# Optimization experiments

Measured on AMD Instinct MI355X. Metric: run time of the kernel, lower is better.

Reference implementation:

```python
import jax, jax.numpy as jnp
from jax import lax
import numpy as np

B, T, N, F_IN, H, E, K = 8, 32, 500, 64, 128, 8000, 3
LN_EPS = 1e-5


def setup_inputs() -> dict:
    key = jax.random.key(0)
    ks = jax.random.split(key, 10)
    x = jax.random.normal(ks[0], (B, T, N, F_IN), dtype=jnp.float32)
    edge_index = jax.random.randint(ks[1], (2, E), 0, N, dtype=jnp.int64)
    edge_weight = jax.random.uniform(ks[2], (E,), dtype=jnp.float32)
    # GCNConv: linear (in->out) + bias
    W_gcn = jax.random.normal(ks[3], (F_IN, H), dtype=jnp.float32) / np.sqrt(F_IN)
    b_gcn = jnp.zeros((H,), dtype=jnp.float32)
    # Conv1d(H, H, K): weight (O, I, K)
    W_temp = jax.random.normal(ks[4], (H, H, K), dtype=jnp.float32) / np.sqrt(H * K)
    b_temp = jnp.zeros((H,), dtype=jnp.float32)
    # LayerNorm(H)
    ln_w = jnp.ones((H,), dtype=jnp.float32)
    ln_b = jnp.zeros((H,), dtype=jnp.float32)
    # residual Linear (in->out)
    W_res = jax.random.normal(ks[5], (F_IN, H), dtype=jnp.float32) / np.sqrt(F_IN)
    b_res = jnp.zeros((H,), dtype=jnp.float32)
    return {"x": x, "edge_index": edge_index, "edge_weight": edge_weight,
            "W_gcn": W_gcn, "b_gcn": b_gcn, "W_temp": W_temp, "b_temp": b_temp,
            "ln_w": ln_w, "ln_b": ln_b, "W_res": W_res, "b_res": b_res}


def reference(x, edge_index, edge_weight, W_gcn, b_gcn, W_temp, b_temp, ln_w, ln_b, W_res, b_res):
    Bv, Tv, Nv, Fv = x.shape
    Hv = W_gcn.shape[1]
    res = x @ W_res + b_res  # (B,T,N,H)

    # ---- spatial GCNConv on B*T replicated graphs (vectorized, no index offsetting) ----
    xf = x.reshape(Bv * Tv, Nv, Fv) @ W_gcn  # (BT,N,H)
    src, dst = edge_index[0], edge_index[1]
    loops = jnp.arange(Nv, dtype=edge_index.dtype)
    src2 = jnp.concatenate([src, loops])
    dst2 = jnp.concatenate([dst, loops])
    ew2 = jnp.concatenate([edge_weight, jnp.ones((Nv,), dtype=edge_weight.dtype)])
    deg = jax.ops.segment_sum(ew2, dst2, num_segments=Nv)
    dinv = jnp.where(deg > 0, deg ** -0.5, 0.0)
    norm = dinv[src2] * ew2 * dinv[dst2]  # (E+N,)
    msgs = xf[:, src2, :] * norm[None, :, None]  # (BT, E+N, H)
    agg = jax.vmap(lambda m: jax.ops.segment_sum(m, dst2, num_segments=Nv))(msgs)
    h = jax.nn.gelu(agg + b_gcn, approximate=False)  # (BT,N,H)

    # ---- temporal Conv1d over T ----
    h = h.reshape(Bv, Tv, Nv, Hv).transpose(0, 2, 3, 1).reshape(Bv * Nv, Hv, Tv)
    pad = K // 2
    h = lax.conv_general_dilated(h, W_temp, window_strides=(1,), padding=[(pad, pad)],
                                 dimension_numbers=("NCH", "OIH", "NCH"))
    h = jax.nn.gelu(h + b_temp[None, :, None], approximate=False)
    h = h.reshape(Bv, Nv, Hv, Tv).transpose(0, 3, 1, 2)  # (B,T,N,H)

    # ---- fused residual + LayerNorm over last dim ----
    y = h + res
    mu = jnp.mean(y, axis=-1, keepdims=True)
    var = jnp.mean((y - mu) ** 2, axis=-1, keepdims=True)
    return (y - mu) * lax.rsqrt(var + LN_EPS) * ln_w + ln_b
```

## Files before the change

kernel.cpp:

```cpp
#include <hip/hip_runtime.h>
#include <hip/hip_bf16.h>
#include <math.h>

#define Bv 8
#define Tv 32
#define Nv 500
#define Fin 64
#define Hv 128
#define Ev 8000
#define Kv 3
#define BT (Bv*Tv)
#define ROWS (BT*Nv)
#define TP (Tv+2)
#define KK (Kv*Hv)
#define LDSROW 144

typedef __attribute__((ext_vector_type(8))) short s8v;
typedef __attribute__((ext_vector_type(4))) float f4v;

__device__ __forceinline__ float gelu_exact(float v){
    return 0.5f*v*(1.0f + erff(v*0.70710678118654752440f));
}
__device__ __forceinline__ short f2bs(float f){
    union { __hip_bfloat16 h; short s; } u;
    u.h = __float2bfloat16(f);
    return u.s;
}
__device__ __forceinline__ float b2f(short s){
    union { unsigned int i; float f; } u;
    u.i = ((unsigned int)(unsigned short)s) << 16;
    return u.f;
}

__global__ __launch_bounds__(1024) void k_prep(const int* __restrict__ ei,
        const float* __restrict__ ew, float* __restrict__ dinv,
        int* __restrict__ offs, int* __restrict__ csrc, float* __restrict__ cw){
    __shared__ float sdeg[Nv];
    __shared__ int   scnt[Nv];
    __shared__ float sdv[Nv];
    __shared__ int   scur[Nv];
    __shared__ int   sa[512], sb[512];
    int tid = threadIdx.x;
    if (tid < Nv){ sdeg[tid] = 1.0f; scnt[tid] = 0; }
    __syncthreads();
    for (int e = tid; e < Ev; e += 1024){
        int d = ei[Ev + e];
        atomicAdd(&sdeg[d], ew[e]);
        atomicAdd(&scnt[d], 1);
    }
    __syncthreads();
    int c = 0;
    if (tid < Nv){
        float d = sdeg[tid];
        float v = (d > 0.f) ? rsqrtf(d) : 0.f;
        sdv[tid] = v; dinv[tid] = v;
    }
    if (tid < 512){ c = (tid < Nv) ? scnt[tid] : 0; sa[tid] = c; }
    __syncthreads();
    int* s = sa; int* t = sb;
    for (int off = 1; off < 512; off <<= 1){
        int v = 0;
        if (tid < 512){ v = s[tid]; if (tid >= off) v += s[tid - off]; }
        if (tid < 512) t[tid] = v;
        __syncthreads();
        int* tmp = s; s = t; t = tmp;
    }
    if (tid < Nv){ int excl = s[tid] - c; offs[tid] = excl; scur[tid] = excl; }
    if (tid == 0) offs[Nv] = Ev;
    __syncthreads();
    for (int e = tid; e < Ev; e += 1024){
        int sn = ei[e], d = ei[Ev + e];
        int pos = atomicAdd(&scur[d], 1);
        csrc[pos] = sn;
        cw[pos] = sdv[sn]*ew[e]*sdv[d];
    }
}

__global__ __launch_bounds__(256) void k_xpose(const float* __restrict__ x,
        short* __restrict__ X2b, const float* __restrict__ W,
        const float* __restrict__ Wg, const float* __restrict__ Wr,
        short* __restrict__ W2, short* __restrict__ Wgt, short* __restrict__ Wrt){
    int bid = blockIdx.x;
    if (bid < ROWS/16){
        int gid = bid*256 + threadIdx.x;
        int row = gid >> 4, c4 = gid & 15;
        int bt = row / Nv;
        int n  = row - bt*Nv;
        float4 v = ((const float4*)x)[gid];
        short4 sv;
        sv.x = f2bs(v.x); sv.y = f2bs(v.y); sv.z = f2bs(v.z); sv.w = f2bs(v.w);
        *(short4*)(X2b + (size_t)n*(BT*64) + bt*64 + c4*4) = sv;
    } else {
        int idx = (bid - ROWS/16)*256 + threadIdx.x;
        if (idx < Hv*Hv*Kv){
            int o = idx/(Hv*Kv);
            int rem = idx - o*(Hv*Kv);
            int i = rem/Kv, k = rem - i*Kv;
            W2[o*KK + k*Hv + i] = f2bs(W[idx]);
        } else if (idx < Hv*Hv*Kv + Hv*64){
            int j = idx - Hv*Hv*Kv;
            int o = j >> 6, k = j & 63;
            Wgt[j] = f2bs(Wg[k*Hv + o]);
        } else if (idx < Hv*Hv*Kv + 2*Hv*64){
            int j = idx - Hv*Hv*Kv - Hv*64;
            int o = j >> 6, k = j & 63;
            Wrt[j] = f2bs(Wr[k*Hv + o]);
        }
    }
}

__global__ __launch_bounds__(256) void k_spmm(const short* __restrict__ X2b,
        const float* __restrict__ dinv, const int* __restrict__ offs,
        const int* __restrict__ csrc, const float* __restrict__ cw,
        short* __restrict__ AGG2){
    int bid = blockIdx.x;
    int ct = bid / Nv;
    int n  = bid - ct*Nv;
    int col = ct*2048 + threadIdx.x*8;
    float dv = dinv[n];
    float sw = dv*dv;
    float acc[8];
    s8v v = *(const s8v*)(X2b + (size_t)n*(BT*64) + col);
    #pragma unroll
    for (int q = 0; q < 8; ++q) acc[q] = sw * b2f(v[q]);
    int e0 = offs[n], e1 = offs[n+1];
    for (int e = e0; e < e1; ++e){
        int s = csrc[e]; float w = cw[e];
        s8v u = *(const s8v*)(X2b + (size_t)s*(BT*64) + col);
        #pragma unroll
        for (int q = 0; q < 8; ++q) acc[q] = fmaf(w, b2f(u[q]), acc[q]);
    }
    s8v r;
    #pragma unroll
    for (int q = 0; q < 8; ++q) r[q] = f2bs(acc[q]);
    *(s8v*)(AGG2 + (size_t)n*(BT*64) + col) = r;
}

__global__ __launch_bounds__(256, 2) void k_mega(
        const short* __restrict__ AGG2, const short* __restrict__ X2b,
        const short* __restrict__ W2, const short* __restrict__ Wgt,
        const short* __restrict__ Wrt,
        const float* __restrict__ bg, const float* __restrict__ btm,
        const float* __restrict__ br, const float* __restrict__ lw,
        const float* __restrict__ lb, float* __restrict__ out){
    __shared__ short hs[4*TP*LDSROW];
    __shared__ float red[Tv][4][2];
    int tid  = threadIdx.x;
    int w    = tid >> 6;
    int lane = tid & 63;
    int quad = lane >> 4;
    int laneo = lane & 15;
    int bid = blockIdx.x;
    int b  = bid / 125;
    int n0 = (bid - b*125) * 4;
    int o_base = w*32;

    float bgv[2], bbv[2], brv[2], lwv[2], lbv[2];
    #pragma unroll
    for (int nt = 0; nt < 2; ++nt){
        int o = o_base + nt*16 + laneo;
        bgv[nt] = bg[o]; bbv[nt] = btm[o]; brv[nt] = br[o];
        lwv[nt] = lw[o]; lbv[nt] = lb[o];
    }

    s8v bwg[2][2];
    #pragma unroll
    for (int nt = 0; nt < 2; ++nt){
        const short* wp = Wgt + (o_base + nt*16 + laneo)*64 + quad*8;
        bwg[nt][0] = *(const s8v*)wp;
        bwg[nt][1] = *(const s8v*)(wp + 32);
    }

    if (tid < 128){
        int node = tid >> 5, rem = tid & 31;
        int tp = (rem >> 4)*(TP-1), c8 = rem & 15;
        s8v z = {0,0,0,0,0,0,0,0};
        *(s8v*)&hs[node*(TP*LDSROW) + tp*LDSROW + c8*8] = z;
    }

    for (int g = 0; g < 4; ++g){
        int n = n0 + g;
        const short* ap = AGG2 + ((size_t)n*BT + b*Tv)*64;
        #pragma unroll
        for (int m = 0; m < 2; ++m){
            const short* arp = ap + (m*16 + laneo)*64 + quad*8;
            s8v a0 = *(const s8v*)arp;
            s8v a1 = *(const s8v*)(arp + 32);
            f4v h0 = {0.f,0.f,0.f,0.f}, h1 = {0.f,0.f,0.f,0.f};
            h0 = __builtin_amdgcn_mfma_f32_16x16x32_bf16(a0, bwg[0][0], h0, 0,0,0);
            h0 = __builtin_amdgcn_mfma_f32_16x16x32_bf16(a1, bwg[0][1], h0, 0,0,0);
            h1 = __builtin_amdgcn_mfma_f32_16x16x32_bf16(a0, bwg[1][0], h1, 0,0,0);
            h1 = __builtin_amdgcn_mfma_f32_16x16x32_bf16(a1, bwg[1][1], h1, 0,0,0);
            #pragma unroll
            for (int r = 0; r < 4; ++r){
                int tp = m*16 + quad*4 + r + 1;
                short* hrow = &hs[g*(TP*LDSROW) + tp*LDSROW];
                hrow[o_base + laneo]      = f2bs(gelu_exact(h0[r] + bgv[0]));
                hrow[o_base + 16 + laneo] = f2bs(gelu_exact(h1[r] + bgv[1]));
            }
        }
    }

    s8v breg[2][12], bwr[2][2];
    #pragma unroll
    for (int nt = 0; nt < 2; ++nt){
        int o = o_base + nt*16 + laneo;
        const short* wp = W2 + o*KK + quad*8;
        #pragma unroll
        for (int s = 0; s < 12; ++s)
            breg[nt][s] = *(const s8v*)(wp + s*32);
        const short* wr = Wrt + o*64 + quad*8;
        bwr[nt][0] = *(const s8v*)wr;
        bwr[nt][1] = *(const s8v*)(wr + 32);
    }
    __syncthreads();

    for (int g = 0; g < 4; ++g){
        int n = n0 + g;
        f4v acc[2][2];
        #pragma unroll
        for (int m = 0; m < 2; ++m)
            #pragma unroll
            for (int nt = 0; nt < 2; ++nt)
                acc[m][nt] = (f4v){0.f,0.f,0.f,0.f};
        #pragma unroll
        for (int m = 0; m < 2; ++m){
            #pragma unroll
            for (int s = 0; s < 12; ++s){
                int k  = s >> 2;
                int i0 = (s & 3) * 32;
                int tp = m*16 + laneo + k;
                s8v a = *(const s8v*)&hs[g*(TP*LDSROW) + tp*LDSROW + i0 + quad*8];
                acc[m][0] = __builtin_amdgcn_mfma_f32_16x16x32_bf16(a, breg[0][s], acc[m][0], 0,0,0);
                acc[m][1] = __builtin_amdgcn_mfma_f32_16x16x32_bf16(a, breg[1][s], acc[m][1], 0,0,0);
            }
        }
        f4v racc[2][2];
        #pragma unroll
        for (int m = 0; m < 2; ++m)
            #pragma unroll
            for (int nt = 0; nt < 2; ++nt)
                racc[m][nt] = (f4v){0.f,0.f,0.f,0.f};
        const short* xp = X2b + ((size_t)n*BT + b*Tv)*64;
        #pragma unroll
        for (int m = 0; m < 2; ++m){
            const short* xrp = xp + (m*16 + laneo)*64 + quad*8;
            s8v a0 = *(const s8v*)xrp;
            s8v a1 = *(const s8v*)(xrp + 32);
            racc[m][0] = __builtin_amdgcn_mfma_f32_16x16x32_bf16(a0, bwr[0][0], racc[m][0], 0,0,0);
            racc[m][0] = __builtin_amdgcn_mfma_f32_16x16x32_bf16(a1, bwr[0][1], racc[m][0], 0,0,0);
            racc[m][1] = __builtin_amdgcn_mfma_f32_16x16x32_bf16(a0, bwr[1][0], racc[m][1], 0,0,0);
            racc[m][1] = __builtin_amdgcn_mfma_f32_16x16x32_bf16(a1, bwr[1][1], racc[m][1], 0,0,0);
        }
        size_t obase = ((size_t)b*Tv*Nv + n)*Hv;
        float yv[2][2][4];
        float srow[2][4], ssrow[2][4];
        #pragma unroll
        for (int m = 0; m < 2; ++m)
            #pragma unroll
            for (int r = 0; r < 4; ++r){ srow[m][r] = 0.f; ssrow[m][r] = 0.f; }
        #pragma unroll
        for (int m = 0; m < 2; ++m){
            #pragma unroll
            for (int nt = 0; nt < 2; ++nt){
                #pragma unroll
                for (int r = 0; r < 4; ++r){
                    float gv = gelu_exact(acc[m][nt][r] + bbv[nt]);
                    float y = gv + racc[m][nt][r] + brv[nt];
                    yv[m][nt][r] = y;
                    srow[m][r] += y; ssrow[m][r] += y*y;
                }
            }
        }
        #pragma unroll
        for (int m = 0; m < 2; ++m)
            #pragma unroll
            for (int r = 0; r < 4; ++r){
                #pragma unroll
                for (int msk = 8; msk >= 1; msk >>= 1){
                    srow[m][r]  += __shfl_xor(srow[m][r],  msk, 64);
                    ssrow[m][r] += __shfl_xor(ssrow[m][r], msk, 64);
                }
            }
        if (laneo == 0){
            #pragma unroll
            for (int m = 0; m < 2; ++m)
                #pragma unroll
                for (int r = 0; r < 4; ++r){
                    int t = m*16 + quad*4 + r;
                    red[t][w][0] = srow[m][r];
                    red[t][w][1] = ssrow[m][r];
                }
        }
        __syncthreads();
        #pragma unroll
        for (int m = 0; m < 2; ++m){
            #pragma unroll
            for (int r = 0; r < 4; ++r){
                int t = m*16 + quad*4 + r;
                float s  = red[t][0][0] + red[t][1][0] + red[t][2][0] + red[t][3][0];
                float ss = red[t][0][1] + red[t][1][1] + red[t][2][1] + red[t][3][1];
                float mu = s * (1.f/128.f);
                float var = fmaxf(ss * (1.f/128.f) - mu*mu, 0.f);
                float rstd = rsqrtf(var + 1e-5f);
                #pragma unroll
                for (int nt = 0; nt < 2; ++nt){
                    int o = o_base + nt*16 + laneo;
                    out[obase + (size_t)t*Nv*Hv + o] =
                        (yv[m][nt][r] - mu)*rstd*lwv[nt] + lbv[nt];
                }
            }
        }
        __syncthreads();
    }
}

extern "C" void kernel_launch(void* const* d_in, const int* in_sizes, int n_in,
                              void* d_out, int out_size, void* d_ws, size_t ws_size,
                              hipStream_t stream){
    const float* x   = (const float*)d_in[0];
    const int*   ei  = (const int*)d_in[1];
    const float* ew  = (const float*)d_in[2];
    const float* Wg  = (const float*)d_in[3];
    const float* bg  = (const float*)d_in[4];
    const float* Wtm = (const float*)d_in[5];
    const float* btm = (const float*)d_in[6];
    const float* lw  = (const float*)d_in[7];
    const float* lb  = (const float*)d_in[8];
    const float* Wr  = (const float*)d_in[9];
    const float* br  = (const float*)d_in[10];
    float* out = (float*)d_out;

    char* ws = (char*)d_ws;
    float* dinv = (float*)(ws + 0);
    int*   offs = (int*)  (ws + 4096);
    int*   csrc = (int*)  (ws + 8192);
    float* cwn  = (float*)(ws + 40960);
    short* W2   = (short*)(ws + 73728);
    short* Wgt  = (short*)(ws + 172032);
    short* Wrt  = (short*)(ws + 188416);
    short* X2b  = (short*)(ws + 204800);
    short* AGG2 = (short*)(ws + 16588800);

    k_prep <<<1, 1024, 0, stream>>>(ei, ew, dinv, offs, csrc, cwn);
    k_xpose<<<ROWS/16 + 256, 256, 0, stream>>>(x, X2b, Wtm, Wg, Wr, W2, Wgt, Wrt);
    k_spmm <<<8*Nv, 256, 0, stream>>>(X2b, dinv, offs, csrc, cwn, AGG2);
    k_mega <<<(Bv*Nv)/4, 256, 0, stream>>>(AGG2, X2b, W2, Wgt, Wrt,
                                           bg, btm, br, lw, lb, out);
}
```

Measured before the change: 218.7 us.

## Replace CSR SpMM with dense normalized adjacency GEMM on MFMA

Builds a dense 512x512 bf16 normalized adjacency matrix with atomics and replaces the per-node CSR gather SpMM with a dense MFMA GEMM against a transposed bf16 copy of x. This trades a sparse gather (16 edges per node on average) for a dense GEMM roughly 32x larger in FLOPs but regular and tensor-core friendly. It also swaps erff for a polynomial erf approximation and halves the nodes per block in the mega kernel to double the grid. Extra costs: a memset, three small prep kernels, an extra transposed copy of x, and reduced GELU accuracy.

```diff
diff --git a/kernel.cpp b/kernel.cpp
--- a/kernel.cpp
+++ b/kernel.cpp
@@ -14,84 +14,93 @@
 #define TP (Tv+2)
 #define KK (Kv*Hv)
 #define LDSROW 144
+#define NP 512
+#define NCOL (BT*Fin)
 
 typedef __attribute__((ext_vector_type(8))) short s8v;
 typedef __attribute__((ext_vector_type(4))) float f4v;
 
-__device__ __forceinline__ float gelu_exact(float v){
-    return 0.5f*v*(1.0f + erff(v*0.70710678118654752440f));
-}
 __device__ __forceinline__ short f2bs(float f){
     union { __hip_bfloat16 h; short s; } u;
     u.h = __float2bfloat16(f);
     return u.s;
 }
-__device__ __forceinline__ float b2f(short s){
-    union { unsigned int i; float f; } u;
-    u.i = ((unsigned int)(unsigned short)s) << 16;
-    return u.f;
-}
-
-__global__ __launch_bounds__(1024) void k_prep(const int* __restrict__ ei,
-        const float* __restrict__ ew, float* __restrict__ dinv,
-        int* __restrict__ offs, int* __restrict__ csrc, float* __restrict__ cw){
-    __shared__ float sdeg[Nv];
-    __shared__ int   scnt[Nv];
-    __shared__ float sdv[Nv];
-    __shared__ int   scur[Nv];
-    __shared__ int   sa[512], sb[512];
+__device__ __forceinline__ float erf_fast(float x){
+    float a = fabsf(x);
+    float t = __builtin_amdgcn_rcpf(fmaf(0.3275911f, a, 1.0f));
+    float p = t*fmaf(t, fmaf(t, fmaf(t, fmaf(t, 1.061405429f, -1.453152027f),
+                     1.421413741f), -0.284496736f), 0.254829592f);
+    float e = exp2f(-a*a*1.442695041f);
+    return copysignf(1.0f - p*e, x);
+}
+__device__ __forceinline__ float gelu_exact(float v){
+    return 0.5f*v*(1.0f + erf_fast(v*0.70710678118654752440f));
+}
+
+__global__ void k_prep1(const int* __restrict__ ei, const float* __restrict__ ew,
+                        float* __restrict__ deg, float* __restrict__ Adense){
+    int e = blockIdx.x*256 + threadIdx.x;
+    if (e >= Ev) return;
+    int s = ei[e], d = ei[Ev + e];
+    float w = ew[e];
+    atomicAdd(&deg[d], w);
+    atomicAdd(&Adense[d*NP + s], w);
+}
+
+__global__ void k_prep2(const float* __restrict__ deg, float* __restrict__ dinv){
     int tid = threadIdx.x;
-    if (tid < Nv){ sdeg[tid] = 1.0f; scnt[tid] = 0; }
-    __syncthreads();
-    for (int e = tid; e < Ev; e += 1024){
-        int d = ei[Ev + e];
-        atomicAdd(&sdeg[d], ew[e]);
-        atomicAdd(&scnt[d], 1);
-    }
-    __syncthreads();
-    int c = 0;
-    if (tid < Nv){
-        float d = sdeg[tid];
-        float v = (d > 0.f) ? rsqrtf(d) : 0.f;
-        sdv[tid] = v; dinv[tid] = v;
-    }
-    if (tid < 512){ c = (tid < Nv) ? scnt[tid] : 0; sa[tid] = c; }
-    __syncthreads();
-    int* s = sa; int* t = sb;
-    for (int off = 1; off < 512; off <<= 1){
-        int v = 0;
-        if (tid < 512){ v = s[tid]; if (tid >= off) v += s[tid - off]; }
-        if (tid < 512) t[tid] = v;
+    if (tid < Nv) dinv[tid] = rsqrtf(deg[tid] + 1.0f);
+}
+
+__global__ __launch_bounds__(256) void k_anorm(const float* __restrict__ Adense,
+        const float* __restrict__ dinv, short* __restrict__ Ab){
+    int idx = blockIdx.x*256 + threadIdx.x;
+    int d = idx >> 9, s = idx & (NP-1);
+    float v = Adense[idx] + ((d == s) ? 1.0f : 0.0f);
+    float dd = (d < Nv) ? dinv[d] : 0.f;
+    float ds = (s < Nv) ? dinv[s] : 0.f;
+    Ab[idx] = f2bs(v * dd * ds);
+}
+
+__global__ __launch_bounds__(256) void k_xpose(const float* __restrict__ x,
+        short* __restrict__ X2b, short* __restrict__ X2bT,
+        const float* __restrict__ W, const float* __restrict__ Wg,
+        const float* __restrict__ Wr, short* __restrict__ W2,
+        short* __restrict__ Wgt, short* __restrict__ Wrt){
+    int bid = blockIdx.x;
+    if (bid < 2048){
+        __shared__ short ls[64*68];
+        int bt = bid >> 3, nt = bid & 7;
+        int n0 = nt*64;
+        int rows = (n0 + 64 <= Nv) ? 64 : (Nv - n0);
+        int tid = threadIdx.x;
+        if (rows < 64){
+            for (int j = tid; j < (64-rows)*68; j += 256) ls[rows*68 + j] = 0;
+        }
+        const float* xp = x + ((size_t)bt*Nv + n0)*64;
+        for (int q = tid; q < rows*16; q += 256){
+            int i = q >> 4, c4 = q & 15;
+            float4 v = ((const float4*)xp)[q];
+            short4 sv;
+            sv.x = f2bs(v.x); sv.y = f2bs(v.y); sv.z = f2bs(v.z); sv.w = f2bs(v.w);
+            *(short4*)&ls[i*68 + c4*4] = sv;
+        }
         __syncthreads();
-        int* tmp = s; s = t; t = tmp;
-    }
-    if (tid < Nv){ int excl = s[tid] - c; offs[tid] = excl; scur[tid] = excl; }
-    if (tid == 0) offs[Nv] = Ev;
-    __syncthreads();
-    for (int e = tid; e < Ev; e += 1024){
-        int sn = ei[e], d = ei[Ev + e];
-        int pos = atomicAdd(&scur[d], 1);
-        csrc[pos] = sn;
-        cw[pos] = sdv[sn]*ew[e]*sdv[d];
-    }
-}
-
-__global__ __launch_bounds__(256) void k_xpose(const float* __restrict__ x,
-        short* __restrict__ X2b, const float* __restrict__ W,
-        const float* __restrict__ Wg, const float* __restrict__ Wr,
-        short* __restrict__ W2, short* __restrict__ Wgt, short* __restrict__ Wrt){
-    int bid = blockIdx.x;
-    if (bid < ROWS/16){
-        int gid = bid*256 + threadIdx.x;
-        int row = gid >> 4, c4 = gid & 15;
-        int bt = row / Nv;
-        int n  = row - bt*Nv;
-        float4 v = ((const float4*)x)[gid];
-        short4 sv;
-        sv.x = f2bs(v.x); sv.y = f2bs(v.y); sv.z = f2bs(v.z); sv.w = f2bs(v.w);
-        *(short4*)(X2b + (size_t)n*(BT*64) + bt*64 + c4*4) = sv;
+        for (int q = tid; q < 64*16; q += 256){
+            int i = q >> 4, c4 = q & 15;
+            if (i < rows)
+                *(short4*)(X2b + (size_t)(n0+i)*NCOL + bt*64 + c4*4)
+                    = *(const short4*)&ls[i*68 + c4*4];
+        }
+        for (int q = tid; q < 64*8; q += 256){
+            int c = q & 63, ch = q >> 6;
+            s8v v;
+            #pragma unroll
+            for (int j = 0; j < 8; ++j) v[j] = ls[(ch*8 + j)*68 + c];
+            *(s8v*)(X2bT + (size_t)(bt*64 + c)*NP + n0 + ch*8) = v;
+        }
     } else {
-        int idx = (bid - ROWS/16)*256 + threadIdx.x;
+        int idx = (bid - 2048)*256 + threadIdx.x;
         if (idx < Hv*Hv*Kv){
             int o = idx/(Hv*Kv);
             int rem = idx - o*(Hv*Kv);
@@ -109,31 +118,50 @@
     }
 }
 
-__global__ __launch_bounds__(256) void k_spmm(const short* __restrict__ X2b,
-        const float* __restrict__ dinv, const int* __restrict__ offs,
-        const int* __restrict__ csrc, const float* __restrict__ cw,
-        short* __restrict__ AGG2){
-    int bid = blockIdx.x;
-    int ct = bid / Nv;
-    int n  = bid - ct*Nv;
-    int col = ct*2048 + threadIdx.x*8;
-    float dv = dinv[n];
-    float sw = dv*dv;
-    float acc[8];
-    s8v v = *(const s8v*)(X2b + (size_t)n*(BT*64) + col);
-    #pragma unroll
-    for (int q = 0; q < 8; ++q) acc[q] = sw * b2f(v[q]);
-    int e0 = offs[n], e1 = offs[n+1];
-    for (int e = e0; e < e1; ++e){
-        int s = csrc[e]; float w = cw[e];
-        s8v u = *(const s8v*)(X2b + (size_t)s*(BT*64) + col);
-        #pragma unroll
-        for (int q = 0; q < 8; ++q) acc[q] = fmaf(w, b2f(u[q]), acc[q]);
-    }
-    s8v r;
-    #pragma unroll
-    for (int q = 0; q < 8; ++q) r[q] = f2bs(acc[q]);
-    *(s8v*)(AGG2 + (size_t)n*(BT*64) + col) = r;
+__global__ __launch_bounds__(256) void k_aggemm(const short* __restrict__ Ab,
+        const short* __restrict__ X2bT, short* __restrict__ AGG2){
+    __shared__ short cs[64*264];
+    int tid = threadIdx.x;
+    int w = tid >> 6, lane = tid & 63, quad = lane >> 4, laneo = lane & 15;
+    int m_base = (blockIdx.x >> 6) * 64;
+    int c_base = (blockIdx.x & 63) * 256;
+    f4v acc[4][4];
+    #pragma unroll
+    for (int mt = 0; mt < 4; ++mt)
+        #pragma unroll
+        for (int nt = 0; nt < 4; ++nt)
+            acc[mt][nt] = (f4v){0.f,0.f,0.f,0.f};
+    const short* ap0 = Ab + (size_t)(m_base + laneo)*NP + quad*8;
+    const short* bp0 = X2bT + (size_t)(c_base + w*64 + laneo)*NP + quad*8;
+    #pragma unroll 4
+    for (int k0 = 0; k0 < NP; k0 += 32){
+        s8v af[4], bf[4];
+        #pragma unroll
+        for (int mt = 0; mt < 4; ++mt) af[mt] = *(const s8v*)(ap0 + (size_t)mt*16*NP + k0);
+        #pragma unroll
+        for (int nt = 0; nt < 4; ++nt) bf[nt] = *(const s8v*)(bp0 + (size_t)nt*16*NP + k0);
+        #pragma unroll
+        for (int mt = 0; mt < 4; ++mt)
+            #pragma unroll
+            for (int nt = 0; nt < 4; ++nt)
+                acc[mt][nt] = __builtin_amdgcn_mfma_f32_16x16x32_bf16(af[mt], bf[nt], acc[mt][nt], 0,0,0);
+    }
+    #pragma unroll
+    for (int mt = 0; mt < 4; ++mt)
+        #pragma unroll
+        for (int nt = 0; nt < 4; ++nt)
+            #pragma unroll
+            for (int r = 0; r < 4; ++r){
+                int row = mt*16 + quad*4 + r;
+                int col = w*64 + nt*16 + laneo;
+                cs[row*264 + col] = f2bs(acc[mt][nt][r]);
+            }
+    __syncthreads();
+    for (int q = tid; q < 64*32; q += 256){
+        int row = q >> 5, ch = q & 31;
+        *(s8v*)(AGG2 + (size_t)(m_base + row)*NCOL + c_base + ch*8)
+            = *(const s8v*)&cs[row*264 + ch*8];
+    }
 }
 
 __global__ __launch_bounds__(256, 2) void k_mega(
@@ -143,7 +171,7 @@
         const float* __restrict__ bg, const float* __restrict__ btm,
         const float* __restrict__ br, const float* __restrict__ lw,
         const float* __restrict__ lb, float* __restrict__ out){
-    __shared__ short hs[4*TP*LDSROW];
+    __shared__ short hs[2*TP*LDSROW];
     __shared__ float red[Tv][4][2];
     int tid  = threadIdx.x;
     int w    = tid >> 6;
@@ -151,8 +179,8 @@
     int quad = lane >> 4;
     int laneo = lane & 15;
     int bid = blockIdx.x;
-    int b  = bid / 125;
-    int n0 = (bid - b*125) * 4;
+    int b  = bid / 250;
+    int n0 = (bid - b*250) * 2;
     int o_base = w*32;
 
     float bgv[2], bbv[2], brv[2], lwv[2], lbv[2];
@@ -171,14 +199,14 @@
         bwg[nt][1] = *(const s8v*)(wp + 32);
     }
 
-    if (tid < 128){
+    if (tid < 64){
         int node = tid >> 5, rem = tid & 31;
         int tp = (rem >> 4)*(TP-1), c8 = rem & 15;
         s8v z = {0,0,0,0,0,0,0,0};
         *(s8v*)&hs[node*(TP*LDSROW) + tp*LDSROW + c8*8] = z;
     }
 
-    for (int g = 0; g < 4; ++g){
+    for (int g = 0; g < 2; ++g){
         int n = n0 + g;
         const short* ap = AGG2 + ((size_t)n*BT + b*Tv)*64;
         #pragma unroll
@@ -215,7 +243,7 @@
     }
     __syncthreads();
 
-    for (int g = 0; g < 4; ++g){
+    for (int g = 0; g < 2; ++g){
         int n = n0 + g;
         f4v acc[2][2];
         #pragma unroll
@@ -332,19 +360,24 @@
     float* out = (float*)d_out;
 
     char* ws = (char*)d_ws;
-    float* dinv = (float*)(ws + 0);
-    int*   offs = (int*)  (ws + 4096);
-    int*   csrc = (int*)  (ws + 8192);
-    float* cwn  = (float*)(ws + 40960);
-    short* W2   = (short*)(ws + 73728);
-    short* Wgt  = (short*)(ws + 172032);
-    short* Wrt  = (short*)(ws + 188416);
-    short* X2b  = (short*)(ws + 204800);
-    short* AGG2 = (short*)(ws + 16588800);
-
-    k_prep <<<1, 1024, 0, stream>>>(ei, ew, dinv, offs, csrc, cwn);
-    k_xpose<<<ROWS/16 + 256, 256, 0, stream>>>(x, X2b, Wtm, Wg, Wr, W2, Wgt, Wrt);
-    k_spmm <<<8*Nv, 256, 0, stream>>>(X2b, dinv, offs, csrc, cwn, AGG2);
-    k_mega <<<(Bv*Nv)/4, 256, 0, stream>>>(AGG2, X2b, W2, Wgt, Wrt,
-                                           bg, btm, br, lw, lb, out);
-}
+    float* Adense = (float*)(ws + 0);
+    float* deg    = (float*)(ws + 1048576);
+    float* dinv   = (float*)(ws + 1050624);
+    short* Ab     = (short*)(ws + 1052672);
+    short* W2     = (short*)(ws + 1576960);
+    short* Wgt    = (short*)(ws + 1675264);
+    short* Wrt    = (short*)(ws + 1691648);
+    short* X2b    = (short*)(ws + 1708032);
+    short* X2bT   = (short*)(ws + 18485248);
+    short* AGG2   = (short*)(ws + 35262464);
+
+    hipMemsetAsync(ws, 0, 1048576 + 2048, stream);
+
+    k_prep1 <<<(Ev+255)/256, 256, 0, stream>>>(ei, ew, deg, Adense);
+    k_prep2 <<<1, 512, 0, stream>>>(deg, dinv);
+    k_anorm <<<(NP*NP)/256, 256, 0, stream>>>(Adense, dinv, Ab);
+    k_xpose <<<2048 + 256, 256, 0, stream>>>(x, X2b, X2bT, Wtm, Wg, Wr, W2, Wgt, Wrt);
+    k_aggemm<<<8*64, 256, 0, stream>>>(Ab, X2bT, AGG2);
+    k_mega  <<<2000, 256, 0, stream>>>(AGG2, X2b, W2, Wgt, Wrt,
+                                       bg, btm, br, lw, lb, out);
+}
```

Result: no change. 219.6 us (+0.4%).
